# Kernel optimization log

Measured on AMD Instinct MI355X. Metric: run time of the kernel, lower is better.

Reference implementation:

```python
import itertools
import jax, jax.numpy as jnp
import numpy as np

B, N, C, H = 4, 48, 16, 64
CIN = [48, 64, 128, 192]   # per-order MLP input dims after expand/reduce/concat/permute
COUT = 16

def _exclude_mask(n, cnt, dtype):
    # mask[i1..icnt] = 1 iff all object indices are pairwise distinct
    if cnt <= 1:
        return jnp.ones((n,), dtype=dtype)
    idx = [jnp.arange(n).reshape((1,) * d + (n,) + (1,) * (cnt - 1 - d)) for d in range(cnt)]
    m = jnp.ones((n,) * cnt, dtype=bool)
    for a in range(cnt):
        for b in range(a + 1, cnt):
            m = m & (idx[a] != idx[b])
    return m.astype(dtype)

def _reduce(x, dim):
    # x: [B] + [n]*dim + [C]; exists=max / forall=min over last object axis, exclude_self mask
    n = x.shape[1]
    m = _exclude_mask(n, dim, x.dtype)[..., None]  # [n]*dim + [1], broadcasts over B and C
    ex = jnp.max(x * m, axis=-2)
    fa = jnp.min(x * m + (1.0 - m), axis=-2)
    out = jnp.stack([ex, fa], axis=-1)  # interleave (exists, forall) per channel
    return out.reshape(out.shape[:-2] + (out.shape[-2] * 2,))

def _expand(x, dim, n):
    # insert a new object axis at position dim+1 and broadcast to n
    return jnp.broadcast_to(jnp.expand_dims(x, dim + 1), x.shape[:dim + 1] + (n,) + x.shape[dim + 1:])

def _permute(x, dim):
    # concat all permutations of the object axes along channels
    if dim <= 1:
        return x
    parts = [jnp.transpose(x, (0,) + p + (dim + 1,)) for p in itertools.permutations(range(1, dim + 1))]
    return jnp.concatenate(parts, axis=-1)

def _logic(x, W1, b1, W2, b2):
    # LogicInferenceLayer: Linear -> ReLU -> Linear -> Sigmoid on channel axis
    return jax.nn.sigmoid(jax.nn.relu(x @ W1 + b1) @ W2 + b2)

def setup_inputs() -> dict:
    key = jax.random.key(0)
    ks = jax.random.split(key, 24)
    inp = {
        'x0': jax.random.uniform(ks[0], (B, C), dtype=jnp.float32),
        'x1': jax.random.uniform(ks[1], (B, N, C), dtype=jnp.float32),
        'x2': jax.random.uniform(ks[2], (B, N, N, C), dtype=jnp.float32),
        'x3': jax.random.uniform(ks[3], (B, N, N, N, C), dtype=jnp.float32),
    }
    for o, cin in enumerate(CIN):
        inp[f'W1_{o}'] = jax.random.normal(ks[4 + 4 * o], (cin, H), dtype=jnp.float32) * 0.05
        inp[f'b1_{o}'] = jnp.zeros((H,), dtype=jnp.float32)
        inp[f'W2_{o}'] = jax.random.normal(ks[5 + 4 * o], (H, COUT), dtype=jnp.float32) * 0.05
        inp[f'b2_{o}'] = jnp.zeros((COUT,), dtype=jnp.float32)
    return inp

def reference(x0, x1, x2, x3,
              W1_0, b1_0, W2_0, b2_0,
              W1_1, b1_1, W2_1, b2_1,
              W1_2, b1_2, W2_2, b2_2,
              W1_3, b1_3, W2_3, b2_3):
    n = x1.shape[1]
    # order 0: [self, reduce(order1)]
    t0 = jnp.concatenate([x0, _reduce(x1, 1)], axis=-1)
    y0 = _logic(t0, W1_0, b1_0, W2_0, b2_0)
    # order 1: [expand(order0), self, reduce(order2)]
    t1 = jnp.concatenate([_expand(x0, 0, n), x1, _reduce(x2, 2)], axis=-1)
    y1 = _logic(t1, W1_1, b1_1, W2_1, b2_1)
    # order 2: [expand(order1), self, reduce(order3)], permute 2 object axes
    t2 = jnp.concatenate([_expand(x1, 1, n), x2, _reduce(x3, 3)], axis=-1)
    y2 = _logic(_permute(t2, 2), W1_2, b1_2, W2_2, b2_2)
    # order 3 (max order): [expand(order2), self], permute 3 object axes
    t3 = jnp.concatenate([_expand(x2, 2, n), x3], axis=-1)
    y3 = _logic(_permute(t3, 3), W1_3, b1_3, W2_3, b2_3)
    return (y0, y1, y2, y3)
```

## Files before the change

kernel.cpp:

```cpp
#include <hip/hip_runtime.h>
#include <hip/hip_bf16.h>


typedef __bf16 bf16x8 __attribute__((ext_vector_type(8)));
typedef unsigned short us8 __attribute__((ext_vector_type(8)));
typedef float f32x4 __attribute__((ext_vector_type(4)));

#define NPAIR 589824
#define NRED3 294912

__device__ __forceinline__ unsigned short f2bf(float f) {
    __hip_bfloat16 h = __float2bfloat16(f);
    return __builtin_bit_cast(unsigned short, h);
}
__device__ __forceinline__ unsigned int pk2(float a, float b) {
    return (unsigned int)f2bf(a) | ((unsigned int)f2bf(b) << 16);
}
__device__ __forceinline__ float bflo(unsigned int u) {
    return __builtin_bit_cast(float, u << 16);
}
__device__ __forceinline__ float bfhi(unsigned int u) {
    return __builtin_bit_cast(float, u & 0xffff0000u);
}
__device__ __forceinline__ float sigmoidf_(float z) {
    return 1.0f / (1.0f + __expf(-z));
}
__device__ __forceinline__ bf16x8 ld_bf8(const unsigned short* p) {
    return __builtin_bit_cast(bf16x8, *(const us8*)p);
}
__device__ __forceinline__ bf16x8 pack8(float4 a, float4 b) {
    us8 u;
    u[0] = f2bf(a.x); u[1] = f2bf(a.y); u[2] = f2bf(a.z); u[3] = f2bf(a.w);
    u[4] = f2bf(b.x); u[5] = f2bf(b.y); u[6] = f2bf(b.z); u[7] = f2bf(b.w);
    return __builtin_bit_cast(bf16x8, u);
}

__global__ __launch_bounds__(256) void phaseA_kernel(
    const float* __restrict__ x2, const float* __restrict__ W1,
    const float* __restrict__ b1,
    float* __restrict__ wsA, unsigned short* __restrict__ wsB,
    unsigned short* __restrict__ wsC)
{
    __shared__ float xr[4][32];
    const int t = threadIdx.x;
    if (t < 128) {
        const int pr2 = t >> 5, c = t & 31;
        const int gg = blockIdx.x * 4 + pr2;
        const int bb = gg / 2304, pp2 = gg % 2304, P = pp2 / 48, Q = pp2 % 48;
        const float* base = x2 + (size_t)bb * 36864;
        xr[pr2][c] = (c < 16) ? base[(P * 48 + Q) * 16 + c]
                              : base[(Q * 48 + P) * 16 + (c - 16)];
    }
    __syncthreads();
    const int pr = t >> 6, h = t & 63;
    const int g = blockIdx.x * 4 + pr;
    float a = b1[h], bacc = 0.f, cacc = 0.f;
#pragma unroll
    for (int c = 0; c < 16; ++c) {
        const float xpq = xr[pr][c], xqp = xr[pr][16 + c];
        a    += xpq * W1[(  0 + c) * 64 + h] + xqp * W1[( 64 + c) * 64 + h];
        bacc += xpq * W1[( 32 + c) * 64 + h] + xqp * W1[( 96 + c) * 64 + h];
        cacc += xpq * W1[(128 + c) * 64 + h] + xqp * W1[(160 + c) * 64 + h];
    }
    const size_t o = (size_t)g * 64 + h;
    wsA[o] = a;
    wsB[o] = f2bf(bacc);
    wsC[o] = f2bf(cacc);
}

__global__ __launch_bounds__(192, 3) void y3_kernel(
    const float* __restrict__ x3,
    const float* __restrict__ W1, const float* __restrict__ W2,
    const float* __restrict__ b2,
    const float* __restrict__ wsA,
    const unsigned short* __restrict__ wsB,
    const unsigned short* __restrict__ wsC,
    float* __restrict__ out)
{
    __shared__ __align__(16) unsigned short w1t[64 * 104];
    const int t = threadIdx.x;
    const int w = t >> 6, lane = t & 63, lr = lane & 15, lg = lane >> 4;

#pragma unroll
    for (int p = 0; p < 16; ++p) {
        const int e = p * 192 + t;
        const int h = e & 63, kk = (e >> 6) * 2;
        const int r0 = 16 + ((kk >> 4) << 5) + (kk & 15);
        *(unsigned int*)(w1t + h * 104 + kk) =
            pk2(W1[r0 * 64 + h], W1[(r0 + 1) * 64 + h]);
    }
    __syncthreads();

    bf16x8 w1f[4][3];
#pragma unroll
    for (int n = 0; n < 4; ++n)
#pragma unroll
        for (int ks = 0; ks < 3; ++ks)
            w1f[n][ks] = ld_bf8(w1t + (16 * n + lr) * 104 + 32 * ks + 8 * lg);

    bf16x8 w2f[2];
#pragma unroll
    for (int m = 0; m < 2; ++m) {
        us8 u;
#pragma unroll
        for (int e = 0; e < 8; ++e) {
            const int ch = 16 * (e >> 1) + 4 * lg + 2 * (e & 1) + m;
            u[e] = f2bf(W2[ch * 16 + lr]);
        }
        w2f[m] = __builtin_bit_cast(bf16x8, u);
    }
    const float4 b2v = *(const float4*)(b2 + 4 * lg);
    const int row = 16 * w + lr;
    const int c0 = 8 * (lg & 1);
    const bool hi = (lg >> 1) != 0;

    for (int it = 0; it < 4; ++it) {
        const int g = blockIdx.x * 4 + it;
        const int b = g / 2304, pp = g % 2304, i = pp / 48, j = pp % 48;
        const float* xb3 = x3 + (size_t)b * 1769472;
        const int sb0 = i * 36864 + j * 768 + row * 16;
        const int sb1 = i * 36864 + row * 768 + j * 16;
        const int sb2 = j * 36864 + i * 768 + row * 16;
        const int sb3 = row * 36864 + i * 768 + j * 16;
        const int sb4 = j * 36864 + row * 768 + i * 16;
        const int sb5 = row * 36864 + j * 768 + i * 16;
        const float* p0 = xb3 + (hi ? sb1 : sb0) + c0;
        const float* p1 = xb3 + (hi ? sb3 : sb2) + c0;
        const float* p2 = xb3 + (hi ? sb5 : sb4) + c0;
        const bf16x8 xf0 = pack8(*(const float4*)p0, *(const float4*)(p0 + 4));
        const bf16x8 xf1 = pack8(*(const float4*)p1, *(const float4*)(p1 + 4));
        const bf16x8 xf2 = pack8(*(const float4*)p2, *(const float4*)(p2 + 4));

        f32x4 acc[4];
#pragma unroll
        for (int n = 0; n < 4; ++n) {
            acc[n] = f32x4{0.f, 0.f, 0.f, 0.f};
            acc[n] = __builtin_amdgcn_mfma_f32_16x16x32_bf16(w1f[n][0], xf0, acc[n], 0, 0, 0);
            acc[n] = __builtin_amdgcn_mfma_f32_16x16x32_bf16(w1f[n][1], xf1, acc[n], 0, 0, 0);
            acc[n] = __builtin_amdgcn_mfma_f32_16x16x32_bf16(w1f[n][2], xf2, acc[n], 0, 0, 0);
        }
        const size_t baseB = ((size_t)((b * 48 + i) * 48 + row)) * 64 + 4 * lg;
        const size_t baseC = ((size_t)((b * 48 + j) * 48 + row)) * 64 + 4 * lg;
        const size_t baseA = ((size_t)((b * 48 + i) * 48 + j)) * 64 + 4 * lg;
#pragma unroll
        for (int n = 0; n < 4; ++n) {
            const uint2 Bu = *(const uint2*)(wsB + baseB + 16 * n);
            const uint2 Cu = *(const uint2*)(wsC + baseC + 16 * n);
            const float4 Au = *(const float4*)(wsA + baseA + 16 * n);
            acc[n][0] = fmaxf(acc[n][0] + Au.x + bflo(Bu.x) + bflo(Cu.x), 0.f);
            acc[n][1] = fmaxf(acc[n][1] + Au.y + bfhi(Bu.x) + bfhi(Cu.x), 0.f);
            acc[n][2] = fmaxf(acc[n][2] + Au.z + bflo(Bu.y) + bflo(Cu.y), 0.f);
            acc[n][3] = fmaxf(acc[n][3] + Au.w + bfhi(Bu.y) + bfhi(Cu.y), 0.f);
        }
        bf16x8 hf[2];
#pragma unroll
        for (int m = 0; m < 2; ++m) {
            us8 u;
#pragma unroll
            for (int e = 0; e < 8; ++e)
                u[e] = f2bf(acc[e >> 1][2 * (e & 1) + m]);
            hf[m] = __builtin_bit_cast(bf16x8, u);
        }
        f32x4 o2 = {0.f, 0.f, 0.f, 0.f};
        o2 = __builtin_amdgcn_mfma_f32_16x16x32_bf16(w2f[0], hf[0], o2, 0, 0, 0);
        o2 = __builtin_amdgcn_mfma_f32_16x16x32_bf16(w2f[1], hf[1], o2, 0, 0, 0);
        float4 ov;
        ov.x = sigmoidf_(o2[0] + b2v.x);
        ov.y = sigmoidf_(o2[1] + b2v.y);
        ov.z = sigmoidf_(o2[2] + b2v.z);
        ov.w = sigmoidf_(o2[3] + b2v.w);
        *(float4*)(out + (size_t)g * 768 + row * 16 + 4 * lg) = ov;
    }
}

__global__ __launch_bounds__(256) void red3_kernel(
    const float* __restrict__ x3, unsigned short* __restrict__ red3)
{
    const int slot = blockIdx.x * 256 + threadIdx.x;
    const int c = slot & 15;
    const int q = slot >> 4;
    const int j = q % 48, pi = q / 48, i = pi % 48;
    const float* p = x3 + (size_t)q * 768 + c;
    float ex = -__builtin_inff(), fa = __builtin_inff();
    const bool mij = (i != j);
#pragma unroll 8
    for (int k = 0; k < 48; ++k) {
        const bool m = mij & (k != i) & (k != j);
        const float v = p[k * 16];
        ex = fmaxf(ex, m ? v : 0.f);
        fa = fminf(fa, m ? v : 1.f);
    }
    *(unsigned int*)(red3 + (size_t)q * 32 + 2 * c) = pk2(ex, fa);
}

__global__ __launch_bounds__(192, 3) void y2_mlp_kernel(
    const float* __restrict__ x1, const float* __restrict__ x2,
    const float* __restrict__ W1, const float* __restrict__ b1,
    const float* __restrict__ W2, const float* __restrict__ b2,
    const unsigned short* __restrict__ red3, float* __restrict__ out)
{
    __shared__ __align__(16) unsigned short w1t[64 * 136];
    const int t = threadIdx.x;
    const int w = t >> 6, lane = t & 63, lr = lane & 15, lg = lane >> 4;

#pragma unroll
    for (int p = 0; p < 22; ++p) {
        const int e = p * 192 + t;
        if (e < 4096) {
            const int h = e & 63, k2 = e >> 6;
            *(unsigned int*)(w1t + h * 136 + 2 * k2) =
                pk2(W1[(2 * k2) * 64 + h], W1[(2 * k2 + 1) * 64 + h]);
        }
    }
    __syncthreads();

    bf16x8 w1f[4][4];
#pragma unroll
    for (int n = 0; n < 4; ++n)
#pragma unroll
        for (int ks = 0; ks < 4; ++ks)
            w1f[n][ks] = ld_bf8(w1t + (16 * n + lr) * 136 + 32 * ks + 8 * lg);

    bf16x8 w2f[2];
#pragma unroll
    for (int m = 0; m < 2; ++m) {
        us8 u;
#pragma unroll
        for (int e = 0; e < 8; ++e) {
            const int ch = 16 * (e >> 1) + 4 * lg + 2 * (e & 1) + m;
            u[e] = f2bf(W2[ch * 16 + lr]);
        }
        w2f[m] = __builtin_bit_cast(bf16x8, u);
    }
    float4 b1v[4];
#pragma unroll
    for (int n = 0; n < 4; ++n) b1v[n] = *(const float4*)(b1 + 16 * n + 4 * lg);
    const float4 b2v = *(const float4*)(b2 + 4 * lg);

    const int bq = blockIdx.x;
    const int b = bq / 48, i = bq % 48;
    const float* x2b = x2 + (size_t)b * 36864;
    const int row = 16 * w + lr;
    const int j = row;
    const int c0 = 8 * (lg & 1);
    const bool hi = (lg >> 1) != 0;

    const float* a0 = hi ? (x2b + (i * 48 + j) * 16 + c0) : (x1 + (b * 48 + i) * 16 + c0);
    const float* a2 = hi ? (x2b + (j * 48 + i) * 16 + c0) : (x1 + (b * 48 + j) * 16 + c0);
    const unsigned short* r1 = red3 + ((size_t)(b * 48 + i) * 48 + j) * 32 + (hi ? 16 : 0) + c0;
    const unsigned short* r3 = red3 + ((size_t)(b * 48 + j) * 48 + i) * 32 + (hi ? 16 : 0) + c0;

    const bf16x8 xf0 = pack8(*(const float4*)a0, *(const float4*)(a0 + 4));
    const bf16x8 xf1 = ld_bf8(r1);
    const bf16x8 xf2 = pack8(*(const float4*)a2, *(const float4*)(a2 + 4));
    const bf16x8 xf3 = ld_bf8(r3);

    f32x4 acc[4];
#pragma unroll
    for (int n = 0; n < 4; ++n) {
        acc[n] = f32x4{0.f, 0.f, 0.f, 0.f};
        acc[n] = __builtin_amdgcn_mfma_f32_16x16x32_bf16(w1f[n][0], xf0, acc[n], 0, 0, 0);
        acc[n] = __builtin_amdgcn_mfma_f32_16x16x32_bf16(w1f[n][1], xf1, acc[n], 0, 0, 0);
        acc[n] = __builtin_amdgcn_mfma_f32_16x16x32_bf16(w1f[n][2], xf2, acc[n], 0, 0, 0);
        acc[n] = __builtin_amdgcn_mfma_f32_16x16x32_bf16(w1f[n][3], xf3, acc[n], 0, 0, 0);
    }
#pragma unroll
    for (int n = 0; n < 4; ++n) {
        acc[n][0] = fmaxf(acc[n][0] + b1v[n].x, 0.f);
        acc[n][1] = fmaxf(acc[n][1] + b1v[n].y, 0.f);
        acc[n][2] = fmaxf(acc[n][2] + b1v[n].z, 0.f);
        acc[n][3] = fmaxf(acc[n][3] + b1v[n].w, 0.f);
    }
    bf16x8 hf[2];
#pragma unroll
    for (int m = 0; m < 2; ++m) {
        us8 u;
#pragma unroll
        for (int e = 0; e < 8; ++e)
            u[e] = f2bf(acc[e >> 1][2 * (e & 1) + m]);
        hf[m] = __builtin_bit_cast(bf16x8, u);
    }
    f32x4 o2 = {0.f, 0.f, 0.f, 0.f};
    o2 = __builtin_amdgcn_mfma_f32_16x16x32_bf16(w2f[0], hf[0], o2, 0, 0, 0);
    o2 = __builtin_amdgcn_mfma_f32_16x16x32_bf16(w2f[1], hf[1], o2, 0, 0, 0);
    float4 ov;
    ov.x = sigmoidf_(o2[0] + b2v.x);
    ov.y = sigmoidf_(o2[1] + b2v.y);
    ov.z = sigmoidf_(o2[2] + b2v.z);
    ov.w = sigmoidf_(o2[3] + b2v.w);
    *(float4*)(out + ((size_t)bq * 48 + row) * 16 + 4 * lg) = ov;
}

__global__ __launch_bounds__(192, 1) void y01_kernel(
    const float* __restrict__ x0, const float* __restrict__ x1,
    const float* __restrict__ x2,
    const float* __restrict__ W1_0, const float* __restrict__ b1_0,
    const float* __restrict__ W2_0, const float* __restrict__ b2_0,
    const float* __restrict__ W1_1, const float* __restrict__ b1_1,
    const float* __restrict__ W2_1, const float* __restrict__ b2_1,
    float* __restrict__ out)
{
    const int t = threadIdx.x;
    if (blockIdx.x < 4) {
        __shared__ __align__(16) unsigned short w1t[64 * 72];
        __shared__ __align__(16) unsigned short red2l[48 * 32];
        const int b = blockIdx.x;
#pragma unroll
        for (int p = 0; p < 11; ++p) {
            const int e = p * 192 + t;
            if (e < 2048) {
                const int h = e & 63, k2 = e >> 6;
                *(unsigned int*)(w1t + h * 72 + 2 * k2) =
                    pk2(W1_1[(2 * k2) * 64 + h], W1_1[(2 * k2 + 1) * 64 + h]);
            }
        }
        const float* x2b = x2 + (size_t)b * 36864;
#pragma unroll
        for (int s4 = 0; s4 < 4; ++s4) {
            const int s = t + 192 * s4;
            const int i = s >> 4, c = s & 15;
            const float* p = x2b + i * 768 + c;
            float ex = -__builtin_inff(), fa = __builtin_inff();
#pragma unroll 8
            for (int jj = 0; jj < 48; ++jj) {
                const bool m = (jj != i);
                const float v = p[jj * 16];
                ex = fmaxf(ex, m ? v : 0.f);
                fa = fminf(fa, m ? v : 1.f);
            }
            *(unsigned int*)(red2l + i * 32 + 2 * c) = pk2(ex, fa);
        }
        __syncthreads();

        const int w = t >> 6, lane = t & 63, lr = lane & 15, lg = lane >> 4;
        const int i = 16 * w + lr;
        const int rho = b * 48 + i;
        bf16x8 w1f[4][2];
#pragma unroll
        for (int n = 0; n < 4; ++n)
#pragma unroll
            for (int ks = 0; ks < 2; ++ks)
                w1f[n][ks] = ld_bf8(w1t + (16 * n + lr) * 72 + 32 * ks + 8 * lg);
        bf16x8 w2f[2];
#pragma unroll
        for (int m = 0; m < 2; ++m) {
            us8 u;
#pragma unroll
            for (int e = 0; e < 8; ++e) {
                const int ch = 16 * (e >> 1) + 4 * lg + 2 * (e & 1) + m;
                u[e] = f2bf(W2_1[ch * 16 + lr]);
            }
            w2f[m] = __builtin_bit_cast(bf16x8, u);
        }
        float4 b1v[4];
#pragma unroll
        for (int n = 0; n < 4; ++n) b1v[n] = *(const float4*)(b1_1 + 16 * n + 4 * lg);
        const float4 b2v = *(const float4*)(b2_1 + 4 * lg);

        const int c0 = 8 * (lg & 1);
        const float* a0 = (lg < 2) ? (x0 + b * 16 + c0) : (x1 + rho * 16 + c0);
        const bf16x8 xf0 = pack8(*(const float4*)a0, *(const float4*)(a0 + 4));
        const bf16x8 xf1 = ld_bf8(red2l + i * 32 + 8 * lg);

        f32x4 acc[4];
#pragma unroll
        for (int n = 0; n < 4; ++n) {
            acc[n] = f32x4{0.f, 0.f, 0.f, 0.f};
            acc[n] = __builtin_amdgcn_mfma_f32_16x16x32_bf16(w1f[n][0], xf0, acc[n], 0, 0, 0);
            acc[n] = __builtin_amdgcn_mfma_f32_16x16x32_bf16(w1f[n][1], xf1, acc[n], 0, 0, 0);
        }
#pragma unroll
        for (int n = 0; n < 4; ++n) {
            acc[n][0] = fmaxf(acc[n][0] + b1v[n].x, 0.f);
            acc[n][1] = fmaxf(acc[n][1] + b1v[n].y, 0.f);
            acc[n][2] = fmaxf(acc[n][2] + b1v[n].z, 0.f);
            acc[n][3] = fmaxf(acc[n][3] + b1v[n].w, 0.f);
        }
        bf16x8 hf[2];
#pragma unroll
        for (int m = 0; m < 2; ++m) {
            us8 u;
#pragma unroll
            for (int e = 0; e < 8; ++e)
                u[e] = f2bf(acc[e >> 1][2 * (e & 1) + m]);
            hf[m] = __builtin_bit_cast(bf16x8, u);
        }
        f32x4 o2 = {0.f, 0.f, 0.f, 0.f};
        o2 = __builtin_amdgcn_mfma_f32_16x16x32_bf16(w2f[0], hf[0], o2, 0, 0, 0);
        o2 = __builtin_amdgcn_mfma_f32_16x16x32_bf16(w2f[1], hf[1], o2, 0, 0, 0);
        float4 ov;
        ov.x = sigmoidf_(o2[0] + b2v.x);
        ov.y = sigmoidf_(o2[1] + b2v.y);
        ov.z = sigmoidf_(o2[2] + b2v.z);
        ov.w = sigmoidf_(o2[3] + b2v.w);
        *(float4*)(out + 64 + (size_t)rho * 16 + 4 * lg) = ov;
    } else {
        __shared__ float t0l[4][56];
        __shared__ float hl[4][72];
        if (t < 64) {
            const int b = t >> 4, c = t & 15;
            const float* p = x1 + b * 768 + c;
            float ex = -__builtin_inff(), fa = __builtin_inff();
#pragma unroll 8
            for (int n = 0; n < 48; ++n) {
                const float v = p[n * 16];
                ex = fmaxf(ex, v);
                fa = fminf(fa, v);
            }
            t0l[b][c] = x0[b * 16 + c];
            t0l[b][16 + 2 * c] = ex;
            t0l[b][17 + 2 * c] = fa;
        }
        __syncthreads();
        if (t < 64) {
            const int h = t;
            float ac0 = b1_0[h], ac1 = ac0, ac2 = ac0, ac3 = ac0;
#pragma unroll
            for (int c = 0; c < 48; ++c) {
                const float wv = W1_0[c * 64 + h];
                ac0 = fmaf(t0l[0][c], wv, ac0);
                ac1 = fmaf(t0l[1][c], wv, ac1);
                ac2 = fmaf(t0l[2][c], wv, ac2);
                ac3 = fmaf(t0l[3][c], wv, ac3);
            }
            hl[0][h] = fmaxf(ac0, 0.f);
            hl[1][h] = fmaxf(ac1, 0.f);
            hl[2][h] = fmaxf(ac2, 0.f);
            hl[3][h] = fmaxf(ac3, 0.f);
        }
        __syncthreads();
        if (t < 64) {
            const int b = t >> 4, o = t & 15;
            float a = b2_0[o];
#pragma unroll
            for (int h = 0; h < 64; ++h)
                a = fmaf(hl[b][h], W2_0[h * 16 + o], a);
            out[b * 16 + o] = sigmoidf_(a);
        }
    }
}

template <int NK>
__device__ __forceinline__ void mlp_head(
    const unsigned short* lds_in, const unsigned short* lds_w1t,
    const unsigned short* lds_w2t, const float* lds_b1, const float* lds_b2,
    unsigned short* lds_h, float* outp)
{
    constexpr int S = NK * 32 + 8;
    const int t = threadIdx.x;
    const int w = t >> 6, lr = t & 15, lg = (t >> 4) & 3;
    f32x4 acc0 = {0.f, 0.f, 0.f, 0.f};
    f32x4 acc1 = acc0, acc2 = acc0, acc3 = acc0;
    const unsigned short* pa = lds_in + (16 * w + lr) * S + lg * 8;
    const unsigned short* pb = lds_w1t + lr * S + lg * 8;
#pragma unroll
    for (int ks = 0; ks < NK; ++ks) {
        bf16x8 a = ld_bf8(pa + ks * 32);
        acc0 = __builtin_amdgcn_mfma_f32_16x16x32_bf16(a, ld_bf8(pb + 0 * 16 * S + ks * 32), acc0, 0, 0, 0);
        acc1 = __builtin_amdgcn_mfma_f32_16x16x32_bf16(a, ld_bf8(pb + 1 * 16 * S + ks * 32), acc1, 0, 0, 0);
        acc2 = __builtin_amdgcn_mfma_f32_16x16x32_bf16(a, ld_bf8(pb + 2 * 16 * S + ks * 32), acc2, 0, 0, 0);
        acc3 = __builtin_amdgcn_mfma_f32_16x16x32_bf16(a, ld_bf8(pb + 3 * 16 * S + ks * 32), acc3, 0, 0, 0);
    }
    const int hrow = 16 * w + lg * 4;
#pragma unroll
    for (int r = 0; r < 4; ++r) {
        lds_h[(hrow + r) * 72 +  0 + lr] = f2bf(fmaxf(acc0[r] + lds_b1[ 0 + lr], 0.f));
        lds_h[(hrow + r) * 72 + 16 + lr] = f2bf(fmaxf(acc1[r] + lds_b1[16 + lr], 0.f));
        lds_h[(hrow + r) * 72 + 32 + lr] = f2bf(fmaxf(acc2[r] + lds_b1[32 + lr], 0.f));
        lds_h[(hrow + r) * 72 + 48 + lr] = f2bf(fmaxf(acc3[r] + lds_b1[48 + lr], 0.f));
    }
    __syncthreads();
    f32x4 o = {0.f, 0.f, 0.f, 0.f};
#pragma unroll
    for (int ks = 0; ks < 2; ++ks) {
        bf16x8 a = ld_bf8(lds_h + (16 * w + lr) * 72 + ks * 32 + lg * 8);
        bf16x8 b = ld_bf8(lds_w2t + lr * 72 + ks * 32 + lg * 8);
        o = __builtin_amdgcn_mfma_f32_16x16x32_bf16(a, b, o, 0, 0, 0);
    }
    const float b2v = lds_b2[lr];
#pragma unroll
    for (int r = 0; r < 4; ++r)
        outp[(hrow + r) * 16 + lr] = sigmoidf_(o[r] + b2v);
}

__global__ __launch_bounds__(192) void y3_fallback_kernel(
    const float* __restrict__ x2, const float* __restrict__ x3,
    const float* __restrict__ W1, const float* __restrict__ b1,
    const float* __restrict__ W2, const float* __restrict__ b2,
    float* __restrict__ out)
{
    __shared__ __align__(16) unsigned short lds_in[48 * 200];
    __shared__ __align__(16) unsigned short lds_w1t[64 * 200];
    __shared__ __align__(16) unsigned short lds_w2t[16 * 72];
    __shared__ __align__(16) unsigned short lds_h[48 * 72];
    __shared__ float lds_b1[64];
    __shared__ float lds_b2[16];
    const int t = threadIdx.x;
#pragma unroll 4
    for (int p = 0; p < 32; ++p) {
        int e = p * 192 + t;
        int h = e & 63, c2 = e >> 6;
        *(unsigned int*)(lds_w1t + h * 200 + 2 * c2) =
            pk2(W1[(2 * c2) * 64 + h], W1[(2 * c2 + 1) * 64 + h]);
    }
    for (int p = 0; p < 3; ++p) {
        int e = p * 192 + t;
        if (e < 512) {
            int n = e & 15, k2 = e >> 4;
            *(unsigned int*)(lds_w2t + n * 72 + 2 * k2) =
                pk2(W2[(2 * k2) * 16 + n], W2[(2 * k2 + 1) * 16 + n]);
        }
    }
    if (t < 64) lds_b1[t] = b1[t];
    if (t < 16) lds_b2[t] = b2[t];
    const int k = t >> 2, c4 = (t & 3) * 4;
#define STAGE3(PTR, BASE, KSTR, CH) do {                                       \
        const float4 v = *(const float4*)((PTR) + (BASE) + k * (KSTR) + c4);   \
        *(uint2*)(lds_in + k * 200 + (CH) + c4) =                              \
            make_uint2(pk2(v.x, v.y), pk2(v.z, v.w));                          \
    } while (0)
    for (int it = 0; it < 9; ++it) {
        const int g = blockIdx.x * 9 + it;
        const int b = g / 2304, rg = g % 2304, i = rg / 48, j = rg % 48;
        const float* xb2 = x2 + b * 36864;
        const float* xb3 = x3 + b * 1769472;
        __syncthreads();
        STAGE3(xb2, i * 768 + j * 16, 0,       0);
        STAGE3(xb3, i * 36864 + j * 768, 16,   16);
        STAGE3(xb2, i * 768, 16,               32);
        STAGE3(xb3, i * 36864 + j * 16, 768,   48);
        STAGE3(xb2, j * 768 + i * 16, 0,       64);
        STAGE3(xb3, j * 36864 + i * 768, 16,   80);
        STAGE3(xb2, i * 16, 768,               96);
        STAGE3(xb3, i * 768 + j * 16, 36864,   112);
        STAGE3(xb2, j * 768, 16,               128);
        STAGE3(xb3, j * 36864 + i * 16, 768,   144);
        STAGE3(xb2, j * 16, 768,               160);
        STAGE3(xb3, j * 768 + i * 16, 36864,   176);
        __syncthreads();
        mlp_head<6>(lds_in, lds_w1t, lds_w2t, lds_b1, lds_b2, lds_h,
                    out + (size_t)g * 768);
    }
#undef STAGE3
}

__global__ __launch_bounds__(192) void y2_kernel(
    const float* __restrict__ x1, const float* __restrict__ x2,
    const float* __restrict__ x3,
    const float* __restrict__ W1, const float* __restrict__ b1,
    const float* __restrict__ W2, const float* __restrict__ b2,
    float* __restrict__ out)
{
    __shared__ __align__(16) unsigned short lds_in[48 * 136];
    __shared__ __align__(16) unsigned short lds_w1t[64 * 136];
    __shared__ __align__(16) unsigned short lds_w2t[16 * 72];
    __shared__ __align__(16) unsigned short lds_h[48 * 72];
    __shared__ float lds_b1[64];
    __shared__ float lds_b2[16];
    const int t = threadIdx.x;
    const int b = blockIdx.x / 48, i = blockIdx.x % 48;
#pragma unroll 2
    for (int p = 0; p < 22; ++p) {
        int e = p * 192 + t;
        if (e < 4096) {
            int h = e & 63, c2 = e >> 6;
            *(unsigned int*)(lds_w1t + h * 136 + 2 * c2) =
                pk2(W1[(2 * c2) * 64 + h], W1[(2 * c2 + 1) * 64 + h]);
        }
    }
    for (int p = 0; p < 3; ++p) {
        int e = p * 192 + t;
        if (e < 512) {
            int n = e & 15, k2 = e >> 4;
            *(unsigned int*)(lds_w2t + n * 72 + 2 * k2) =
                pk2(W2[(2 * k2) * 16 + n], W2[(2 * k2 + 1) * 16 + n]);
        }
    }
    if (t < 64) lds_b1[t] = b1[t];
    if (t < 16) lds_b2[t] = b2[t];
    const int j = t >> 2, c4 = (t & 3) * 4;
    const float* xb2 = x2 + b * 36864;
#define STAGE2(PTR, BASE, JSTR, CH) do {                                       \
        const float4 v = *(const float4*)((PTR) + (BASE) + j * (JSTR) + c4);   \
        *(uint2*)(lds_in + j * 136 + (CH) + c4) =                              \
            make_uint2(pk2(v.x, v.y), pk2(v.z, v.w));                          \
    } while (0)
    STAGE2(x1, b * 768 + i * 16, 0,  0);
    STAGE2(xb2, i * 768, 16,         16);
    STAGE2(x1, b * 768, 16,          64);
    STAGE2(xb2, i * 16, 768,         80);
#undef STAGE2
    {
        const float* pa = x3 + b * 1769472 + (i * 48 + j) * 768 + c4;
        const float* pb = x3 + b * 1769472 + (j * 48 + i) * 768 + c4;
        float exa[4], faa[4], exb[4], fab[4];
#pragma unroll
        for (int u = 0; u < 4; ++u) {
            exa[u] = -__builtin_inff(); faa[u] = __builtin_inff();
            exb[u] = -__builtin_inff(); fab[u] = __builtin_inff();
        }
        for (int kk = 0; kk < 48; ++kk) {
            const bool m = (i != j) & (i != kk) & (j != kk);
            const float4 va = *(const float4*)(pa + kk * 16);
            const float4 vb = *(const float4*)(pb + kk * 16);
            const float av[4] = {va.x, va.y, va.z, va.w};
            const float bv[4] = {vb.x, vb.y, vb.z, vb.w};
#pragma unroll
            for (int u = 0; u < 4; ++u) {
                exa[u] = fmaxf(exa[u], m ? av[u] : 0.f);
                faa[u] = fminf(faa[u], m ? av[u] : 1.f);
                exb[u] = fmaxf(exb[u], m ? bv[u] : 0.f);
                fab[u] = fminf(fab[u], m ? bv[u] : 1.f);
            }
        }
#pragma unroll
        for (int u = 0; u < 4; ++u) {
            const int c = c4 + u;
            *(unsigned int*)(lds_in + j * 136 + 32 + 2 * c) = pk2(exa[u], faa[u]);
            *(unsigned int*)(lds_in + j * 136 + 96 + 2 * c) = pk2(exb[u], fab[u]);
        }
    }
    __syncthreads();
    mlp_head<4>(lds_in, lds_w1t, lds_w2t, lds_b1, lds_b2, lds_h,
                out + (size_t)blockIdx.x * 768);
}

extern "C" void kernel_launch(void* const* d_in, const int* in_sizes, int n_in,
                              void* d_out, int out_size, void* d_ws, size_t ws_size,
                              hipStream_t stream) {
    (void)in_sizes; (void)n_in; (void)out_size;
    const float* x0 = (const float*)d_in[0];
    const float* x1 = (const float*)d_in[1];
    const float* x2 = (const float*)d_in[2];
    const float* x3 = (const float*)d_in[3];
    const float* W1_0 = (const float*)d_in[4];
    const float* b1_0 = (const float*)d_in[5];
    const float* W2_0 = (const float*)d_in[6];
    const float* b2_0 = (const float*)d_in[7];
    const float* W1_1 = (const float*)d_in[8];
    const float* b1_1 = (const float*)d_in[9];
    const float* W2_1 = (const float*)d_in[10];
    const float* b2_1 = (const float*)d_in[11];
    const float* W1_2 = (const float*)d_in[12];
    const float* b1_2 = (const float*)d_in[13];
    const float* W2_2 = (const float*)d_in[14];
    const float* b2_2 = (const float*)d_in[15];
    const float* W1_3 = (const float*)d_in[16];
    const float* b1_3 = (const float*)d_in[17];
    const float* W2_3 = (const float*)d_in[18];
    const float* b2_3 = (const float*)d_in[19];
    float* out = (float*)d_out;

    const size_t ws_need = (size_t)8 * NPAIR + (size_t)2 * NRED3;
    if (ws_size >= ws_need) {
        float* wsA = (float*)d_ws;
        unsigned short* wsB = (unsigned short*)d_ws + 2 * NPAIR;
        unsigned short* wsC = wsB + NPAIR;
        unsigned short* red3 = (unsigned short*)d_ws + 4 * NPAIR;
        phaseA_kernel<<<2304, 256, 0, stream>>>(x2, W1_3, b1_3, wsA, wsB, wsC);
        y3_kernel<<<2304, 192, 0, stream>>>(x3, W1_3, W2_3, b2_3,
                                            wsA, wsB, wsC, out + 150592);
        red3_kernel<<<576, 256, 0, stream>>>(x3, red3);
        y2_mlp_kernel<<<192, 192, 0, stream>>>(x1, x2, W1_2, b1_2, W2_2, b2_2,
                                               red3, out + 3136);
    } else {
        y3_fallback_kernel<<<1024, 192, 0, stream>>>(x2, x3, W1_3, b1_3, W2_3, b2_3,
                                                     out + 150592);
        y2_kernel<<<192, 192, 0, stream>>>(x1, x2, x3, W1_2, b1_2, W2_2, b2_2,
                                           out + 3136);
    }
    y01_kernel<<<5, 192, 0, stream>>>(x0, x1, x2, W1_0, b1_0, W2_0, b2_0,
                                      W1_1, b1_1, W2_1, b2_1, out);
}
```

Baseline: 199.3 us.

## Pre-permute x3 into three bf16 layouts so y3 loads are contiguous

```diff
diff --git a/kernel.cpp b/kernel.cpp
--- a/kernel.cpp
+++ b/kernel.cpp
@@ -8,6 +8,7 @@
 
 #define NPAIR 589824
 #define NRED3 294912
+#define NX3   7077888
 
 __device__ __forceinline__ unsigned short f2bf(float f) {
     __hip_bfloat16 h = __float2bfloat16(f);
@@ -33,6 +34,22 @@
     u[0] = f2bf(a.x); u[1] = f2bf(a.y); u[2] = f2bf(a.z); u[3] = f2bf(a.w);
     u[4] = f2bf(b.x); u[5] = f2bf(b.y); u[6] = f2bf(b.z); u[7] = f2bf(b.w);
     return __builtin_bit_cast(bf16x8, u);
+}
+
+__global__ __launch_bounds__(192) void perm3_kernel(
+    const float* __restrict__ x3,
+    unsigned short* __restrict__ X0, unsigned short* __restrict__ XA,
+    unsigned short* __restrict__ XB)
+{
+    const int g = blockIdx.x;
+    const int m2 = g % 48, t1 = g / 48, m1 = t1 % 48, b = t1 / 48;
+    const int t = threadIdx.x;
+    const int m3 = t >> 2, cq = (t & 3) * 4;
+    const float4 v = *(const float4*)(x3 + (size_t)g * 768 + m3 * 16 + cq);
+    const uint2 u = make_uint2(pk2(v.x, v.y), pk2(v.z, v.w));
+    *(uint2*)(X0 + (size_t)g * 768 + m3 * 16 + cq) = u;
+    *(uint2*)(XA + (((size_t)(b * 48 + m1) * 48 + m3) * 48 + m2) * 16 + cq) = u;
+    *(uint2*)(XB + (((size_t)(b * 48 + m2) * 48 + m3) * 48 + m1) * 16 + cq) = u;
 }
 
 __global__ __launch_bounds__(256) void phaseA_kernel(
@@ -69,6 +86,108 @@
 }
 
 __global__ __launch_bounds__(192, 3) void y3_kernel(
+    const unsigned short* __restrict__ X0,
+    const unsigned short* __restrict__ XA,
+    const unsigned short* __restrict__ XB,
+    const float* __restrict__ W1, const float* __restrict__ W2,
+    const float* __restrict__ b2,
+    const float* __restrict__ wsA,
+    const unsigned short* __restrict__ wsB,
+    const unsigned short* __restrict__ wsC,
+    float* __restrict__ out)
+{
+    __shared__ __align__(16) unsigned short w1t[64 * 104];
+    const int t = threadIdx.x;
+    const int w = t >> 6, lane = t & 63, lr = lane & 15, lg = lane >> 4;
+
+#pragma unroll
+    for (int p = 0; p < 16; ++p) {
+        const int e = p * 192 + t;
+        const int h = e & 63, kk = (e >> 6) * 2;
+        const int r0 = 16 + ((kk >> 4) << 5) + (kk & 15);
+        *(unsigned int*)(w1t + h * 104 + kk) =
+            pk2(W1[r0 * 64 + h], W1[(r0 + 1) * 64 + h]);
+    }
+    __syncthreads();
+
+    bf16x8 w1f[4][3];
+#pragma unroll
+    for (int n = 0; n < 4; ++n)
+#pragma unroll
+        for (int ks = 0; ks < 3; ++ks)
+            w1f[n][ks] = ld_bf8(w1t + (16 * n + lr) * 104 + 32 * ks + 8 * lg);
+
+    bf16x8 w2f[2];
+#pragma unroll
+    for (int m = 0; m < 2; ++m) {
+        us8 u;
+#pragma unroll
+        for (int e = 0; e < 8; ++e) {
+            const int ch = 16 * (e >> 1) + 4 * lg + 2 * (e & 1) + m;
+            u[e] = f2bf(W2[ch * 16 + lr]);
+        }
+        w2f[m] = __builtin_bit_cast(bf16x8, u);
+    }
+    const float4 b2v = *(const float4*)(b2 + 4 * lg);
+    const int row = 16 * w + lr;
+    const int roff = row * 16 + 8 * (lg & 1);
+    const bool hi = (lg >> 1) != 0;
+
+    for (int it = 0; it < 4; ++it) {
+        const int g = blockIdx.x * 4 + it;
+        const int b = g / 2304, pp = g % 2304, i = pp / 48, j = pp % 48;
+        const size_t blkIJ = ((size_t)(b * 48 + i) * 48 + j) * 768;
+        const size_t blkJI = ((size_t)(b * 48 + j) * 48 + i) * 768;
+        const unsigned short* p0 = (hi ? XA + blkIJ : X0 + blkIJ) + roff;
+        const unsigned short* p1 = (hi ? XB + blkIJ : X0 + blkJI) + roff;
+        const unsigned short* p2 = (hi ? XB + blkJI : XA + blkJI) + roff;
+        const bf16x8 xf0 = ld_bf8(p0);
+        const bf16x8 xf1 = ld_bf8(p1);
+        const bf16x8 xf2 = ld_bf8(p2);
+
+        f32x4 acc[4];
+#pragma unroll
+        for (int n = 0; n < 4; ++n) {
+            acc[n] = f32x4{0.f, 0.f, 0.f, 0.f};
+            acc[n] = __builtin_amdgcn_mfma_f32_16x16x32_bf16(w1f[n][0], xf0, acc[n], 0, 0, 0);
+            acc[n] = __builtin_amdgcn_mfma_f32_16x16x32_bf16(w1f[n][1], xf1, acc[n], 0, 0, 0);
+            acc[n] = __builtin_amdgcn_mfma_f32_16x16x32_bf16(w1f[n][2], xf2, acc[n], 0, 0, 0);
+        }
+        const size_t baseB = ((size_t)((b * 48 + i) * 48 + row)) * 64 + 4 * lg;
+        const size_t baseC = ((size_t)((b * 48 + j) * 48 + row)) * 64 + 4 * lg;
+        const size_t baseA = ((size_t)((b * 48 + i) * 48 + j)) * 64 + 4 * lg;
+#pragma unroll
+        for (int n = 0; n < 4; ++n) {
+            const uint2 Bu = *(const uint2*)(wsB + baseB + 16 * n);
+            const uint2 Cu = *(const uint2*)(wsC + baseC + 16 * n);
+            const float4 Au = *(const float4*)(wsA + baseA + 16 * n);
+            acc[n][0] = fmaxf(acc[n][0] + Au.x + bflo(Bu.x) + bflo(Cu.x), 0.f);
+            acc[n][1] = fmaxf(acc[n][1] + Au.y + bfhi(Bu.x) + bfhi(Cu.x), 0.f);
+            acc[n][2] = fmaxf(acc[n][2] + Au.z + bflo(Bu.y) + bflo(Cu.y), 0.f);
+            acc[n][3] = fmaxf(acc[n][3] + Au.w + bfhi(Bu.y) + bfhi(Cu.y), 0.f);
+        }
+        bf16x8 hf[2];
+#pragma unroll
+        for (int m = 0; m < 2; ++m) {
+            us8 u;
+#pragma unroll
+            for (int e = 0; e < 8; ++e)
+                u[e] = f2bf(acc[e >> 1][2 * (e & 1) + m]);
+            hf[m] = __builtin_bit_cast(bf16x8, u);
+        }
+        f32x4 o2 = {0.f, 0.f, 0.f, 0.f};
+        o2 = __builtin_amdgcn_mfma_f32_16x16x32_bf16(w2f[0], hf[0], o2, 0, 0, 0);
+        o2 = __builtin_amdgcn_mfma_f32_16x16x32_bf16(w2f[1], hf[1], o2, 0, 0, 0);
+        float4 ov;
+        ov.x = sigmoidf_(o2[0] + b2v.x);
+        ov.y = sigmoidf_(o2[1] + b2v.y);
+        ov.z = sigmoidf_(o2[2] + b2v.z);
+        ov.w = sigmoidf_(o2[3] + b2v.w);
+        *(float4*)(out + (size_t)g * 768 + row * 16 + 4 * lg) = ov;
+    }
+}
+
+__global__ __launch_bounds__(192, 3) void y3_gather_kernel(
     const float* __restrict__ x3,
     const float* __restrict__ W1, const float* __restrict__ W2,
     const float* __restrict__ b2,
@@ -80,7 +199,6 @@
     __shared__ __align__(16) unsigned short w1t[64 * 104];
     const int t = threadIdx.x;
     const int w = t >> 6, lane = t & 63, lr = lane & 15, lg = lane >> 4;
-
 #pragma unroll
     for (int p = 0; p < 16; ++p) {
         const int e = p * 192 + t;
@@ -90,14 +208,12 @@
             pk2(W1[r0 * 64 + h], W1[(r0 + 1) * 64 + h]);
     }
     __syncthreads();
-
     bf16x8 w1f[4][3];
 #pragma unroll
     for (int n = 0; n < 4; ++n)
 #pragma unroll
         for (int ks = 0; ks < 3; ++ks)
             w1f[n][ks] = ld_bf8(w1t + (16 * n + lr) * 104 + 32 * ks + 8 * lg);
-
     bf16x8 w2f[2];
 #pragma unroll
     for (int m = 0; m < 2; ++m) {
@@ -113,7 +229,6 @@
     const int row = 16 * w + lr;
     const int c0 = 8 * (lg & 1);
     const bool hi = (lg >> 1) != 0;
-
     for (int it = 0; it < 4; ++it) {
         const int g = blockIdx.x * 4 + it;
         const int b = g / 2304, pp = g % 2304, i = pp / 48, j = pp % 48;
@@ -130,7 +245,6 @@
         const bf16x8 xf0 = pack8(*(const float4*)p0, *(const float4*)(p0 + 4));
         const bf16x8 xf1 = pack8(*(const float4*)p1, *(const float4*)(p1 + 4));
         const bf16x8 xf2 = pack8(*(const float4*)p2, *(const float4*)(p2 + 4));
-
         f32x4 acc[4];
 #pragma unroll
         for (int n = 0; n < 4; ++n) {
@@ -651,15 +765,25 @@
     const float* b2_3 = (const float*)d_in[19];
     float* out = (float*)d_out;
 
-    const size_t ws_need = (size_t)8 * NPAIR + (size_t)2 * NRED3;
-    if (ws_size >= ws_need) {
+    const size_t ws_mid  = (size_t)8 * NPAIR + (size_t)2 * NRED3;
+    const size_t ws_full = ws_mid + (size_t)6 * NX3;
+    if (ws_size >= ws_mid) {
         float* wsA = (float*)d_ws;
         unsigned short* wsB = (unsigned short*)d_ws + 2 * NPAIR;
         unsigned short* wsC = wsB + NPAIR;
         unsigned short* red3 = (unsigned short*)d_ws + 4 * NPAIR;
         phaseA_kernel<<<2304, 256, 0, stream>>>(x2, W1_3, b1_3, wsA, wsB, wsC);
-        y3_kernel<<<2304, 192, 0, stream>>>(x3, W1_3, W2_3, b2_3,
-                                            wsA, wsB, wsC, out + 150592);
+        if (ws_size >= ws_full) {
+            unsigned short* X0 = red3 + NRED3;
+            unsigned short* XA = X0 + NX3;
+            unsigned short* XB = XA + NX3;
+            perm3_kernel<<<9216, 192, 0, stream>>>(x3, X0, XA, XB);
+            y3_kernel<<<2304, 192, 0, stream>>>(X0, XA, XB, W1_3, W2_3, b2_3,
+                                                wsA, wsB, wsC, out + 150592);
+        } else {
+            y3_gather_kernel<<<2304, 192, 0, stream>>>(x3, W1_3, W2_3, b2_3,
+                                                       wsA, wsB, wsC, out + 150592);
+        }
         red3_kernel<<<576, 256, 0, stream>>>(x3, red3);
         y2_mlp_kernel<<<192, 192, 0, stream>>>(x1, x2, W1_2, b1_2, W2_2, b2_2,
                                                red3, out + 3136);
```

Result: slower. 207.1 us (+3.9%).
